# Kernel tuning notes

Hardware: AMD Instinct MI355X
Metric: run time of the kernel (lower is better)

## Reference

```python
import jax, jax.numpy as jnp
import numpy as np

B, S, R, E, H = 2, 2048, 128, 2048, 16
D = E // H  # head_dim = 128


def _ste(x, q):
    # straight-through estimator: forward=q, backward=identity
    return x + jax.lax.stop_gradient(q - x)


def quant_weight(w):
    # BitNet b1.58-style ternary weight quantization with mean-abs scale
    scale = jnp.clip(jnp.mean(jnp.abs(w)), 1e-5, None)
    q = jnp.clip(jnp.round(w / scale), -1.0, 1.0) * scale
    return _ste(w, q)


def quant_act(x):
    # per-token 8-bit absmax activation quantization
    s = 127.0 / jnp.clip(jnp.max(jnp.abs(x), axis=-1, keepdims=True), 1e-5, None)
    q = jnp.clip(jnp.round(x * s), -128.0, 127.0) / s
    return _ste(x, q)


def quantized_linear(x, w):
    # dequantized low-bit matmul: Xq @ Wq^T
    return quant_act(x) @ quant_weight(w).T


def setup_inputs() -> dict:
    key = jax.random.key(0)
    ks = jax.random.split(key, 8)
    sc = 1.0 / np.sqrt(E)
    return {
        "x": jax.random.normal(ks[0], (B, S, E), dtype=jnp.float32),
        "reasoning_tokens": jax.random.normal(ks[1], (B, R, E), dtype=jnp.float32),
        "q_w": jax.random.normal(ks[2], (E, E), dtype=jnp.float32) * sc,
        "k_w": jax.random.normal(ks[3], (E, E), dtype=jnp.float32) * sc,
        "v_w": jax.random.normal(ks[4], (E, E), dtype=jnp.float32) * sc,
        "out_w": jax.random.normal(ks[5], (E, E), dtype=jnp.float32) * sc,
        "out_b": jnp.zeros((E,), dtype=jnp.float32),
    }


def _heads(t):
    b, s, _ = t.shape
    return t.reshape(b, s, H, D).transpose(0, 2, 1, 3)  # [B,H,S,D]


def reference(x, reasoning_tokens, q_w, k_w, v_w, out_w, out_b):
    b, s, e = x.shape
    # quantized QKV projections (dequant + matmul)
    q = _heads(quantized_linear(x, q_w))
    k = _heads(quantized_linear(x, k_w))
    v = _heads(quantized_linear(x, v_w))
    # reasoning tokens go through the UNquantized projections (per source)
    rk = _heads(reasoning_tokens @ k_w.T)
    rv = _heads(reasoning_tokens @ v_w.T)
    k = jnp.concatenate([k, rk], axis=2)  # [B,H,S+R,D]
    v = jnp.concatenate([v, rv], axis=2)
    scores = jnp.einsum('bhqd,bhkd->bhqk', q, k) / np.sqrt(D).astype(np.float32)
    attn = jax.nn.softmax(scores, axis=-1)
    o = jnp.einsum('bhqk,bhkd->bhqd', attn, v)
    o = o.transpose(0, 2, 1, 3).reshape(b, s, e)
    return o @ out_w.T + out_b
```

## Files before the change

kernel.cpp:

```cpp
#include <hip/hip_runtime.h>


typedef __bf16 bf16;
typedef __bf16 bf16x8 __attribute__((ext_vector_type(8)));
typedef float  f32x4  __attribute__((ext_vector_type(4)));

#define B_   2
#define S_   2048
#define R_   128
#define E_   2048
#define H_   16
#define D_   128
#define NKV  2176
#define NTOK 4096
#define MTOT 4352
#define KDIM 2048

typedef const __attribute__((address_space(1))) void* gas_ptr;
typedef __attribute__((address_space(3))) void*       las_ptr;

__device__ __forceinline__ void load_lds16(const void* g, void* l) {
  __builtin_amdgcn_global_load_lds((gas_ptr)g, (las_ptr)l, 16, 0, 0);
}

__global__ __launch_bounds__(256) void abs_sum_k(
    const float* __restrict__ w0, const float* __restrict__ w1,
    const float* __restrict__ w2, double* wsD) {
  int z = blockIdx.y;
  const float* w = z == 0 ? w0 : (z == 1 ? w1 : w2);
  int tid = threadIdx.x;
  size_t base = ((size_t)blockIdx.x * 256 + tid) * 8;
  f32x4 a = *(const f32x4*)(w + base);
  f32x4 b = *(const f32x4*)(w + base + 4);
  float s = 0.f;
#pragma unroll
  for (int j = 0; j < 4; j++) s += fabsf(a[j]) + fabsf(b[j]);
  double d = (double)s;
#pragma unroll
  for (int m = 1; m < 64; m <<= 1) d += __shfl_xor(d, m);
  __shared__ double red[4];
  if ((tid & 63) == 0) red[tid >> 6] = d;
  __syncthreads();
  if (tid == 0) atomicAdd(&wsD[z], red[0] + red[1] + red[2] + red[3]);
}

__global__ __launch_bounds__(256) void ternary_k(
    const float* __restrict__ w0, const float* __restrict__ w1,
    const float* __restrict__ w2, const double* __restrict__ wsD, float* wsF,
    bf16* __restrict__ t0, bf16* __restrict__ t1, bf16* __restrict__ t2) {
  int z = blockIdx.y;
  const float* w = z == 0 ? w0 : (z == 1 ? w1 : w2);
  bf16* t        = z == 0 ? t0 : (z == 1 ? t1 : t2);
  float scale = (float)fmax(wsD[z] * (1.0 / 4194304.0), 1e-5);
  if (blockIdx.x == 0 && threadIdx.x == 0) wsF[z] = scale;
  size_t base = ((size_t)blockIdx.x * 256 + threadIdx.x) * 8;
  f32x4 a = *(const f32x4*)(w + base);
  f32x4 b = *(const f32x4*)(w + base + 4);
  float rs = 1.0f / scale;
  bf16x8 o;
#pragma unroll
  for (int j = 0; j < 8; j++) {
    float v = j < 4 ? a[j] : b[j - 4];
    float q = rintf(v * rs);
    q = fminf(fmaxf(q, -1.f), 1.f);
    o[j] = (bf16)q;
  }
  *(bf16x8*)(t + base) = o;
}

__global__ __launch_bounds__(256) void actq_k(
    const float* __restrict__ x, bf16* __restrict__ xq,
    float* __restrict__ aScale) {
  int row = blockIdx.x, tid = threadIdx.x;
  const float* xr = x + (size_t)row * E_;
  f32x4 a = *(const f32x4*)(xr + tid * 8);
  f32x4 b = *(const f32x4*)(xr + tid * 8 + 4);
  float am = 0.f;
#pragma unroll
  for (int j = 0; j < 4; j++) am = fmaxf(am, fmaxf(fabsf(a[j]), fabsf(b[j])));
#pragma unroll
  for (int m = 1; m < 64; m <<= 1) am = fmaxf(am, __shfl_xor(am, m));
  __shared__ float red[4];
  if ((tid & 63) == 0) red[tid >> 6] = am;
  __syncthreads();
  float mx = fmaxf(fmaxf(red[0], red[1]), fmaxf(red[2], red[3]));
  float maxC = fmaxf(mx, 1e-5f);
  float s = 127.0f / maxC;
  bf16x8 o;
#pragma unroll
  for (int j = 0; j < 8; j++) {
    float v = j < 4 ? a[j] : b[j - 4];
    float q = rintf(v * s);
    q = fminf(fmaxf(q, -128.f), 127.f);
    o[j] = (bf16)q;
  }
  *(bf16x8*)(xq + (size_t)row * E_ + tid * 8) = o;
  if (tid == 0) aScale[row] = maxC / 127.0f;
}

__global__ __launch_bounds__(256) void cvt_k(const float* __restrict__ src,
                                             bf16* __restrict__ dst) {
  size_t i = ((size_t)blockIdx.x * 256 + threadIdx.x) * 8;
  f32x4 a = *(const f32x4*)(src + i);
  f32x4 b = *(const f32x4*)(src + i + 4);
  bf16x8 o;
#pragma unroll
  for (int j = 0; j < 4; j++) { o[j] = (bf16)a[j]; o[j + 4] = (bf16)b[j]; }
  *(bf16x8*)(dst + i) = o;
}

__global__ __launch_bounds__(256) void cvt2_k(const float* __restrict__ s0,
                                              const float* __restrict__ s1,
                                              bf16* __restrict__ d0,
                                              bf16* __restrict__ d1) {
  const float* src = blockIdx.y ? s1 : s0;
  bf16* dst = blockIdx.y ? d1 : d0;
  size_t i = ((size_t)blockIdx.x * 256 + threadIdx.x) * 8;
  f32x4 a = *(const f32x4*)(src + i);
  f32x4 b = *(const f32x4*)(src + i + 4);
  bf16x8 o;
#pragma unroll
  for (int j = 0; j < 4; j++) { o[j] = (bf16)a[j]; o[j + 4] = (bf16)b[j]; }
  *(bf16x8*)(dst + i) = o;
}

__global__ __launch_bounds__(256) void cvt_rt_k(const float* __restrict__ rt,
                                                bf16* __restrict__ dst,
                                                float* __restrict__ asc) {
  int row = blockIdx.x;
  size_t base = (size_t)row * E_;
  int t = threadIdx.x;
  f32x4 a = *(const f32x4*)(rt + base + t * 8);
  f32x4 b = *(const f32x4*)(rt + base + t * 8 + 4);
  bf16x8 o;
#pragma unroll
  for (int j = 0; j < 4; j++) { o[j] = (bf16)a[j]; o[j + 4] = (bf16)b[j]; }
  *(bf16x8*)(dst + (size_t)(NTOK + row) * E_ + t * 8) = o;
  if (t == 0) asc[NTOK + row] = 1.0f;
}

__device__ __forceinline__ void gemm_core(const bf16* Arow, const bf16* Brow,
                                          bf16* As, bf16* Bs, int tid,
                                          f32x4 acc[4][4]) {
  int wave = tid >> 6, lane = tid & 63, quad = lane >> 4, l16 = lane & 15;
  int wm = wave >> 1, wn = wave & 1;
  const char* aT = (const char*)Arow;
  const char* bT = (const char*)Brow;
  int c1 = tid + 256;
  size_t aO0 = (size_t)(tid >> 2) * (KDIM * 2) + (size_t)(tid & 3) * 16;
  size_t aO1 = (size_t)(c1 >> 2) * (KDIM * 2) + (size_t)(c1 & 3) * 16;
  char* AsB = (char*)As;
  char* BsB = (char*)Bs;
  int wofs = wave * 1024;
  for (int k0 = 0; k0 < KDIM; k0 += 32) {
    __syncthreads();
    load_lds16(aT + aO0, AsB + wofs);
    load_lds16(aT + aO1, AsB + 4096 + wofs);
    load_lds16(bT + aO0, BsB + wofs);
    load_lds16(bT + aO1, BsB + 4096 + wofs);
    aT += 64;
    bT += 64;
    __syncthreads();
    bf16x8 af[4], bfr[4];
#pragma unroll
    for (int mt = 0; mt < 4; mt++)
      af[mt] = *(const bf16x8*)(As + (wm * 64 + mt * 16 + l16) * 32 + quad * 8);
#pragma unroll
    for (int nt = 0; nt < 4; nt++)
      bfr[nt] = *(const bf16x8*)(Bs + (wn * 64 + nt * 16 + l16) * 32 + quad * 8);
#pragma unroll
    for (int mt = 0; mt < 4; mt++)
#pragma unroll
      for (int nt = 0; nt < 4; nt++)
        acc[mt][nt] = __builtin_amdgcn_mfma_f32_16x16x32_bf16(
            af[mt], bfr[nt], acc[mt][nt], 0, 0, 0);
  }
}

__global__ __launch_bounds__(256) void gemm_qk(
    const bf16* __restrict__ XQR, const bf16* __restrict__ TQ,
    const bf16* __restrict__ TK, const bf16* __restrict__ KWb,
    const float* __restrict__ asc, const float* __restrict__ wsF,
    bf16* __restrict__ QB, bf16* __restrict__ KB) {
  __shared__ bf16 As[128 * 32];
  __shared__ bf16 Bs[128 * 32];
  int m0 = blockIdx.x * 128, n0 = blockIdx.y * 128;
  bool isQ = n0 < 2048;
  bool isRsn = m0 >= NTOK;
  if (isQ && isRsn) return;
  int tid = threadIdx.x;
  int lane = tid & 63, quad = lane >> 4, l16 = lane & 15;
  int wm = (tid >> 6) >> 1, wn = (tid >> 6) & 1;

  const bf16* Bm = isQ ? (TQ + (size_t)n0 * KDIM)
                       : (isRsn ? (KWb + (size_t)(n0 - 2048) * KDIM)
                                : (TK + (size_t)(n0 - 2048) * KDIM));
  float sW = isQ ? wsF[0] : (isRsn ? 1.0f : wsF[1]);

  f32x4 acc[4][4];
  const f32x4 fz = {0.f, 0.f, 0.f, 0.f};
#pragma unroll
  for (int i = 0; i < 4; i++)
#pragma unroll
    for (int j = 0; j < 4; j++) acc[i][j] = fz;
  gemm_core(XQR + (size_t)m0 * KDIM, Bm, As, Bs, tid, acc);

#pragma unroll
  for (int mt = 0; mt < 4; mt++) {
    int mB = m0 + wm * 64 + mt * 16 + quad * 4;
#pragma unroll
    for (int nt = 0; nt < 4; nt++) {
      int n = n0 + wn * 64 + nt * 16 + l16;
      int nn = n & 2047, h = nn >> 7, d = nn & 127;
#pragma unroll
      for (int r = 0; r < 4; r++) {
        int m = mB + r;
        float v = acc[mt][nt][r] * asc[m] * sW;
        int tb, ts;
        if (isRsn) { int j = m - NTOK; tb = j >> 7; ts = 2048 + (j & 127); }
        else       { tb = m >> 11; ts = m & 2047; }
        if (isQ)
          QB[((size_t)((tb * 16 + h) * S_ + ts)) * 128 + d] = (bf16)v;
        else
          KB[((size_t)((tb * 16 + h) * NKV + ts)) * 128 + d] = (bf16)v;
      }
    }
  }
}

__global__ __launch_bounds__(256) void gemm_vt(
    const bf16* __restrict__ TV, const bf16* __restrict__ VWb,
    const bf16* __restrict__ XQR, const float* __restrict__ asc,
    const float* __restrict__ wsF, bf16* __restrict__ VT) {
  __shared__ bf16 As[128 * 32];
  __shared__ bf16 Bs[128 * 32];
  int m0 = blockIdx.x * 128, n0 = blockIdx.y * 128;
  bool isRsn = n0 >= NTOK;
  int tid = threadIdx.x;
  int lane = tid & 63, quad = lane >> 4, l16 = lane & 15;
  int wm = (tid >> 6) >> 1, wn = (tid >> 6) & 1;

  const bf16* Am = (isRsn ? VWb : TV) + (size_t)m0 * KDIM;
  float sW = isRsn ? 1.0f : wsF[2];

  f32x4 acc[4][4];
  const f32x4 fz = {0.f, 0.f, 0.f, 0.f};
#pragma unroll
  for (int i = 0; i < 4; i++)
#pragma unroll
    for (int j = 0; j < 4; j++) acc[i][j] = fz;
  gemm_core(Am, XQR + (size_t)n0 * KDIM, As, Bs, tid, acc);

#pragma unroll
  for (int mt = 0; mt < 4; mt++) {
    int mB = m0 + wm * 64 + mt * 16 + quad * 4;
#pragma unroll
    for (int nt = 0; nt < 4; nt++) {
      int n = n0 + wn * 64 + nt * 16 + l16;
      float sb = asc[n] * sW;
      int tb, ts;
      if (isRsn) { int j = n - NTOK; tb = j >> 7; ts = 2048 + (j & 127); }
      else       { tb = n >> 11; ts = n & 2047; }
#pragma unroll
      for (int r = 0; r < 4; r++) {
        int m = mB + r, h = m >> 7, d = m & 127;
        VT[((size_t)((tb * 16 + h) * 128 + d)) * NKV + ts] =
            (bf16)(acc[mt][nt][r] * sb);
      }
    }
  }
}

__global__ __launch_bounds__(256) void gemm_out(
    const bf16* __restrict__ A, const bf16* __restrict__ Bm,
    const float* __restrict__ bias, float* __restrict__ out) {
  __shared__ bf16 As[128 * 32];
  __shared__ bf16 Bs[128 * 32];
  int m0 = blockIdx.x * 128, n0 = blockIdx.y * 128;
  int tid = threadIdx.x;
  int lane = tid & 63, quad = lane >> 4, l16 = lane & 15;
  int wm = (tid >> 6) >> 1, wn = (tid >> 6) & 1;

  f32x4 acc[4][4];
  const f32x4 fz = {0.f, 0.f, 0.f, 0.f};
#pragma unroll
  for (int i = 0; i < 4; i++)
#pragma unroll
    for (int j = 0; j < 4; j++) acc[i][j] = fz;
  gemm_core(A + (size_t)m0 * KDIM, Bm + (size_t)n0 * KDIM, As, Bs, tid, acc);

#pragma unroll
  for (int mt = 0; mt < 4; mt++) {
    int mB = m0 + wm * 64 + mt * 16 + quad * 4;
#pragma unroll
    for (int nt = 0; nt < 4; nt++) {
      int n = n0 + wn * 64 + nt * 16 + l16;
      float bv = bias[n];
#pragma unroll
      for (int r = 0; r < 4; r++)
        out[(size_t)(mB + r) * E_ + n] = acc[mt][nt][r] + bv;
    }
  }
}

__global__ __launch_bounds__(256) void attn_k(
    const bf16* __restrict__ q, const bf16* __restrict__ k,
    const bf16* __restrict__ vt, bf16* __restrict__ o) {
  __shared__ bf16 Ks[64 * 128];
  __shared__ bf16 Vs[128 * 64];
  __shared__ bf16 Ps[128 * 64];
  const float SC = 0.08838834764831845f;
  const float SHIFT = 12.0f;
  int tid = threadIdx.x;
  int wave = tid >> 6, lane = tid & 63, quad = lane >> 4, l16 = lane & 15;
  int bh = blockIdx.y, q0 = blockIdx.x * 128;

  const bf16* qb = q + ((size_t)bh * S_ + q0) * D_;
  const char* kb = (const char*)(k + (size_t)bh * NKV * D_);
  const char* vb = (const char*)(vt + (size_t)bh * D_ * NKV);

  bf16x8 qf[2][4];
#pragma unroll
  for (int qt = 0; qt < 2; qt++)
#pragma unroll
    for (int ds = 0; ds < 4; ds++)
      qf[qt][ds] = *(const bf16x8*)(qb +
                   (size_t)(wave * 32 + qt * 16 + l16) * D_ + ds * 32 + quad * 8);

  const f32x4 fz = {0.f, 0.f, 0.f, 0.f};
  f32x4 oa[2][8];
#pragma unroll
  for (int i = 0; i < 2; i++)
#pragma unroll
    for (int j = 0; j < 8; j++) oa[i][j] = fz;
  float lsum[2][4];
#pragma unroll
  for (int i = 0; i < 2; i++)
#pragma unroll
    for (int r = 0; r < 4; r++) lsum[i][r] = 0.f;

  char* KsB = (char*)Ks;
  char* VsB = (char*)Vs;
  char* PsB = (char*)Ps;

  int kRow[4], kC[4], vRow[4], vC[4];
#pragma unroll
  for (int i = 0; i < 4; i++) {
    int slot = i * 256 + tid;
    kRow[i] = slot >> 4;
    kC[i] = (slot & 15) ^ (kRow[i] & 15);
    vRow[i] = slot >> 3;
    vC[i] = (slot & 7) ^ (vRow[i] & 7);
  }
  int wofs = wave * 1024;

  for (int kv = 0; kv < NKV; kv += 64) {
    __syncthreads();
#pragma unroll
    for (int i = 0; i < 4; i++)
      load_lds16(kb + (size_t)(kv + kRow[i]) * 256 + kC[i] * 16,
                 KsB + i * 4096 + wofs);
#pragma unroll
    for (int i = 0; i < 4; i++)
      load_lds16(vb + (size_t)vRow[i] * (NKV * 2) + (size_t)kv * 2 + vC[i] * 16,
                 VsB + i * 4096 + wofs);
    __syncthreads();

    f32x4 s[2][4];
#pragma unroll
    for (int i = 0; i < 2; i++)
#pragma unroll
      for (int j = 0; j < 4; j++) s[i][j] = fz;
#pragma unroll
    for (int ds = 0; ds < 4; ds++) {
      bf16x8 kf[4];
#pragma unroll
      for (int kt = 0; kt < 4; kt++) {
        int row = kt * 16 + l16;
        int c = (ds * 4 + quad) ^ (row & 15);
        kf[kt] = *(const bf16x8*)(KsB + row * 256 + c * 16);
      }
#pragma unroll
      for (int qt = 0; qt < 2; qt++)
#pragma unroll
        for (int kt = 0; kt < 4; kt++)
          s[qt][kt] = __builtin_amdgcn_mfma_f32_16x16x32_bf16(
              qf[qt][ds], kf[kt], s[qt][kt], 0, 0, 0);
    }

#pragma unroll
    for (int qt = 0; qt < 2; qt++)
#pragma unroll
      for (int kt = 0; kt < 4; kt++)
#pragma unroll
        for (int r = 0; r < 4; r++)
          s[qt][kt][r] = __expf(s[qt][kt][r] * SC - SHIFT);
#pragma unroll
    for (int qt = 0; qt < 2; qt++)
#pragma unroll
      for (int r = 0; r < 4; r++)
        lsum[qt][r] += (s[qt][0][r] + s[qt][1][r]) + (s[qt][2][r] + s[qt][3][r]);

#pragma unroll
    for (int qt = 0; qt < 2; qt++)
#pragma unroll
      for (int kt = 0; kt < 4; kt++)
#pragma unroll
        for (int r = 0; r < 4; r++) {
          int row = wave * 32 + qt * 16 + quad * 4 + r;
          int col = kt * 16 + l16;
          int c = (col >> 3) ^ (row & 7);
          *(bf16*)(PsB + row * 128 + c * 16 + (col & 7) * 2) =
              (bf16)s[qt][kt][r];
        }
    __syncthreads();

#pragma unroll
    for (int ks = 0; ks < 2; ks++) {
      bf16x8 pf[2], vf[8];
#pragma unroll
      for (int qt = 0; qt < 2; qt++) {
        int row = wave * 32 + qt * 16 + l16;
        int c = (ks * 4 + quad) ^ (row & 7);
        pf[qt] = *(const bf16x8*)(PsB + row * 128 + c * 16);
      }
#pragma unroll
      for (int dt = 0; dt < 8; dt++) {
        int row = dt * 16 + l16;
        int c = (ks * 4 + quad) ^ (row & 7);
        vf[dt] = *(const bf16x8*)(VsB + row * 128 + c * 16);
      }
#pragma unroll
      for (int qt = 0; qt < 2; qt++)
#pragma unroll
        for (int dt = 0; dt < 8; dt++)
          oa[qt][dt] = __builtin_amdgcn_mfma_f32_16x16x32_bf16(
              pf[qt], vf[dt], oa[qt][dt], 0, 0, 0);
    }
  }

  int b = bh >> 4, h = bh & 15;
#pragma unroll
  for (int qt = 0; qt < 2; qt++) {
    float rl[4];
#pragma unroll
    for (int r = 0; r < 4; r++) {
      float l = lsum[qt][r];
#pragma unroll
      for (int msk = 1; msk < 16; msk <<= 1) l += __shfl_xor(l, msk);
      rl[r] = 1.0f / l;
    }
#pragma unroll
    for (int dt = 0; dt < 8; dt++)
#pragma unroll
      for (int r = 0; r < 4; r++) {
        int srow = q0 + wave * 32 + qt * 16 + quad * 4 + r;
        int col = h * 128 + dt * 16 + l16;
        o[((size_t)(b * S_ + srow)) * E_ + col] = (bf16)(oa[qt][dt][r] * rl[r]);
      }
  }
}

static constexpr size_t O_ASC  = 256;
static constexpr size_t O_XQR  = 32768;
static constexpr size_t SZ_XQR = (size_t)MTOT * E_ * 2;
static constexpr size_t SZ_W   = (size_t)E_ * E_ * 2;
static constexpr size_t O_TQ   = O_XQR + SZ_XQR;
static constexpr size_t O_TK   = O_TQ + SZ_W;
static constexpr size_t O_TV   = O_TK + SZ_W;
static constexpr size_t O_KWB  = O_TV + SZ_W;
static constexpr size_t O_VWB  = O_KWB + SZ_W;
static constexpr size_t O_QB   = O_VWB + SZ_W;
static constexpr size_t SZ_QB  = (size_t)B_ * H_ * S_ * D_ * 2;
static constexpr size_t O_KB   = O_QB + SZ_QB;
static constexpr size_t SZ_KB  = (size_t)B_ * H_ * NKV * D_ * 2;
static constexpr size_t O_VT   = O_KB + SZ_KB;
static constexpr size_t O_OB   = O_TQ;
static constexpr size_t O_OWB  = O_KWB;
static constexpr size_t WS_NEED = O_VT + SZ_KB;

extern "C" void kernel_launch(void* const* d_in, const int* in_sizes, int n_in,
                              void* d_out, int out_size, void* d_ws,
                              size_t ws_size, hipStream_t stream) {
  const float* x  = (const float*)d_in[0];
  const float* rt = (const float*)d_in[1];
  const float* qw = (const float*)d_in[2];
  const float* kw = (const float*)d_in[3];
  const float* vw = (const float*)d_in[4];
  const float* ow = (const float*)d_in[5];
  const float* ob = (const float*)d_in[6];
  char* ws = (char*)d_ws;
  if (ws_size < WS_NEED) return;

  double* wsD = (double*)ws;
  float* wsF  = (float*)(ws + 64);
  float* asc  = (float*)(ws + O_ASC);
  bf16* XQR = (bf16*)(ws + O_XQR);
  bf16* TQ  = (bf16*)(ws + O_TQ);
  bf16* TK  = (bf16*)(ws + O_TK);
  bf16* TV  = (bf16*)(ws + O_TV);
  bf16* KWb = (bf16*)(ws + O_KWB);
  bf16* VWb = (bf16*)(ws + O_VWB);
  bf16* QB  = (bf16*)(ws + O_QB);
  bf16* KB  = (bf16*)(ws + O_KB);
  bf16* VT  = (bf16*)(ws + O_VT);
  bf16* OB  = (bf16*)(ws + O_OB);
  bf16* OWb = (bf16*)(ws + O_OWB);
  float* out = (float*)d_out;

  hipMemsetAsync(ws, 0, 64, stream);
  abs_sum_k<<<dim3(2048, 3), 256, 0, stream>>>(qw, kw, vw, wsD);
  ternary_k<<<dim3(2048, 3), 256, 0, stream>>>(qw, kw, vw, wsD, wsF, TQ, TK, TV);
  actq_k<<<4096, 256, 0, stream>>>(x, XQR, asc);
  cvt_rt_k<<<256, 256, 0, stream>>>(rt, XQR, asc);
  cvt2_k<<<dim3(2048, 2), 256, 0, stream>>>(kw, vw, KWb, VWb);

  gemm_qk<<<dim3(34, 32), 256, 0, stream>>>(XQR, TQ, TK, KWb, asc, wsF, QB, KB);
  cvt_k<<<2048, 256, 0, stream>>>(ow, OWb);
  gemm_vt<<<dim3(16, 34), 256, 0, stream>>>(TV, VWb, XQR, asc, wsF, VT);

  attn_k<<<dim3(16, 32), 256, 0, stream>>>(QB, KB, VT, OB);

  gemm_out<<<dim3(32, 16), 256, 0, stream>>>(OB, OWb, ob, out);
}
```

Before: 581.5 us.

## Use int8 MFMA for quantized QKV projections and fuse prep kernels

Quantized activations and ternary weights are now stored as int8 instead of bf16, and the quantized Q/K/V projections use the i8 16x16x64 MFMA with a swizzled LDS layout, which halves operand bytes and doubles the k-step per instruction. Reasoning-token projections keep a separate bf16 path since they are unquantized. The weight ternarization and all fp32-to-bf16 conversions are merged into one prep kernel, cutting launches. Exactness relies on int32 accumulation of integer products, which matches the dequantized reference up to rounding order.

```diff
diff --git a/kernel.cpp b/kernel.cpp
--- a/kernel.cpp
+++ b/kernel.cpp
@@ -4,6 +4,8 @@
 typedef __bf16 bf16;
 typedef __bf16 bf16x8 __attribute__((ext_vector_type(8)));
 typedef float  f32x4  __attribute__((ext_vector_type(4)));
+typedef int    i32x4  __attribute__((ext_vector_type(4)));
+typedef char   char8  __attribute__((ext_vector_type(8)));
 
 #define B_   2
 #define S_   2048
@@ -13,7 +15,6 @@
 #define D_   128
 #define NKV  2176
 #define NTOK 4096
-#define MTOT 4352
 #define KDIM 2048
 
 typedef const __attribute__((address_space(1))) void* gas_ptr;
@@ -44,32 +45,48 @@
   if (tid == 0) atomicAdd(&wsD[z], red[0] + red[1] + red[2] + red[3]);
 }
 
-__global__ __launch_bounds__(256) void ternary_k(
-    const float* __restrict__ w0, const float* __restrict__ w1,
-    const float* __restrict__ w2, const double* __restrict__ wsD, float* wsF,
-    bf16* __restrict__ t0, bf16* __restrict__ t1, bf16* __restrict__ t2) {
-  int z = blockIdx.y;
-  const float* w = z == 0 ? w0 : (z == 1 ? w1 : w2);
-  bf16* t        = z == 0 ? t0 : (z == 1 ? t1 : t2);
-  float scale = (float)fmax(wsD[z] * (1.0 / 4194304.0), 1e-5);
-  if (blockIdx.x == 0 && threadIdx.x == 0) wsF[z] = scale;
-  size_t base = ((size_t)blockIdx.x * 256 + threadIdx.x) * 8;
-  f32x4 a = *(const f32x4*)(w + base);
-  f32x4 b = *(const f32x4*)(w + base + 4);
-  float rs = 1.0f / scale;
-  bf16x8 o;
-#pragma unroll
-  for (int j = 0; j < 8; j++) {
-    float v = j < 4 ? a[j] : b[j - 4];
-    float q = rintf(v * rs);
-    q = fminf(fmaxf(q, -1.f), 1.f);
-    o[j] = (bf16)q;
-  }
-  *(bf16x8*)(t + base) = o;
+__global__ __launch_bounds__(256) void prep_k(
+    const float* __restrict__ qw, const float* __restrict__ kw,
+    const float* __restrict__ vw, const float* __restrict__ ow,
+    const float* __restrict__ rt, const double* __restrict__ wsD, float* wsF,
+    char* __restrict__ TQ8, char* __restrict__ TK8, char* __restrict__ TV8,
+    bf16* __restrict__ KWb, bf16* __restrict__ VWb, bf16* __restrict__ OWb,
+    bf16* __restrict__ RTb) {
+  int y = blockIdx.y;
+  if (y < 3) {
+    const float* w = y == 0 ? qw : (y == 1 ? kw : vw);
+    char* t        = y == 0 ? TQ8 : (y == 1 ? TK8 : TV8);
+    float scale = (float)fmax(wsD[y] * (1.0 / 4194304.0), 1e-5);
+    if (blockIdx.x == 0 && threadIdx.x == 0) wsF[y] = scale;
+    size_t base = ((size_t)blockIdx.x * 256 + threadIdx.x) * 8;
+    f32x4 a = *(const f32x4*)(w + base);
+    f32x4 b = *(const f32x4*)(w + base + 4);
+    float rs = 1.0f / scale;
+    char8 o;
+#pragma unroll
+    for (int j = 0; j < 8; j++) {
+      float v = j < 4 ? a[j] : b[j - 4];
+      float q = rintf(v * rs);
+      q = fminf(fmaxf(q, -1.f), 1.f);
+      o[j] = (char)(int)q;
+    }
+    *(char8*)(t + base) = o;
+  } else {
+    if (y == 6 && blockIdx.x >= 256) return;
+    const float* src = y == 3 ? kw : (y == 4 ? vw : (y == 5 ? ow : rt));
+    bf16* dst        = y == 3 ? KWb : (y == 4 ? VWb : (y == 5 ? OWb : RTb));
+    size_t i = ((size_t)blockIdx.x * 256 + threadIdx.x) * 8;
+    f32x4 a = *(const f32x4*)(src + i);
+    f32x4 b = *(const f32x4*)(src + i + 4);
+    bf16x8 o;
+#pragma unroll
+    for (int j = 0; j < 4; j++) { o[j] = (bf16)a[j]; o[j + 4] = (bf16)b[j]; }
+    *(bf16x8*)(dst + i) = o;
+  }
 }
 
 __global__ __launch_bounds__(256) void actq_k(
-    const float* __restrict__ x, bf16* __restrict__ xq,
+    const float* __restrict__ x, char* __restrict__ xq,
     float* __restrict__ aScale) {
   int row = blockIdx.x, tid = threadIdx.x;
   const float* xr = x + (size_t)row * E_;
@@ -86,57 +103,16 @@
   float mx = fmaxf(fmaxf(red[0], red[1]), fmaxf(red[2], red[3]));
   float maxC = fmaxf(mx, 1e-5f);
   float s = 127.0f / maxC;
-  bf16x8 o;
+  char8 o;
 #pragma unroll
   for (int j = 0; j < 8; j++) {
     float v = j < 4 ? a[j] : b[j - 4];
     float q = rintf(v * s);
     q = fminf(fmaxf(q, -128.f), 127.f);
-    o[j] = (bf16)q;
-  }
-  *(bf16x8*)(xq + (size_t)row * E_ + tid * 8) = o;
+    o[j] = (char)(int)q;
+  }
+  *(char8*)(xq + (size_t)row * E_ + tid * 8) = o;
   if (tid == 0) aScale[row] = maxC / 127.0f;
-}
-
-__global__ __launch_bounds__(256) void cvt_k(const float* __restrict__ src,
-                                             bf16* __restrict__ dst) {
-  size_t i = ((size_t)blockIdx.x * 256 + threadIdx.x) * 8;
-  f32x4 a = *(const f32x4*)(src + i);
-  f32x4 b = *(const f32x4*)(src + i + 4);
-  bf16x8 o;
-#pragma unroll
-  for (int j = 0; j < 4; j++) { o[j] = (bf16)a[j]; o[j + 4] = (bf16)b[j]; }
-  *(bf16x8*)(dst + i) = o;
-}
-
-__global__ __launch_bounds__(256) void cvt2_k(const float* __restrict__ s0,
-                                              const float* __restrict__ s1,
-                                              bf16* __restrict__ d0,
-                                              bf16* __restrict__ d1) {
-  const float* src = blockIdx.y ? s1 : s0;
-  bf16* dst = blockIdx.y ? d1 : d0;
-  size_t i = ((size_t)blockIdx.x * 256 + threadIdx.x) * 8;
-  f32x4 a = *(const f32x4*)(src + i);
-  f32x4 b = *(const f32x4*)(src + i + 4);
-  bf16x8 o;
-#pragma unroll
-  for (int j = 0; j < 4; j++) { o[j] = (bf16)a[j]; o[j + 4] = (bf16)b[j]; }
-  *(bf16x8*)(dst + i) = o;
-}
-
-__global__ __launch_bounds__(256) void cvt_rt_k(const float* __restrict__ rt,
-                                                bf16* __restrict__ dst,
-                                                float* __restrict__ asc) {
-  int row = blockIdx.x;
-  size_t base = (size_t)row * E_;
-  int t = threadIdx.x;
-  f32x4 a = *(const f32x4*)(rt + base + t * 8);
-  f32x4 b = *(const f32x4*)(rt + base + t * 8 + 4);
-  bf16x8 o;
-#pragma unroll
-  for (int j = 0; j < 4; j++) { o[j] = (bf16)a[j]; o[j + 4] = (bf16)b[j]; }
-  *(bf16x8*)(dst + (size_t)(NTOK + row) * E_ + t * 8) = o;
-  if (t == 0) asc[NTOK + row] = 1.0f;
 }
 
 __device__ __forceinline__ void gemm_core(const bf16* Arow, const bf16* Brow,
@@ -177,13 +153,52 @@
   }
 }
 
+__device__ __forceinline__ void gemm_core_i8(const char* Arow, const char* Brow,
+                                             char* As, char* Bs, int tid,
+                                             i32x4 acc[4][4]) {
+  int wave = tid >> 6, lane = tid & 63, quad = lane >> 4, l16 = lane & 15;
+  int wm = wave >> 1, wn = wave & 1;
+  int s0 = tid, s1 = tid + 256;
+  int r0 = s0 >> 2, r1 = s1 >> 2;
+  size_t aO0 = (size_t)r0 * KDIM + (size_t)((s0 & 3) ^ (r0 & 3)) * 16;
+  size_t aO1 = (size_t)r1 * KDIM + (size_t)((s1 & 3) ^ (r1 & 3)) * 16;
+  const char* aT = Arow;
+  const char* bT = Brow;
+  int wofs = wave * 1024;
+  int cs = (quad ^ (l16 & 3)) * 16;
+  for (int k0 = 0; k0 < KDIM; k0 += 64) {
+    __syncthreads();
+    load_lds16(aT + aO0, As + wofs);
+    load_lds16(aT + aO1, As + 4096 + wofs);
+    load_lds16(bT + aO0, Bs + wofs);
+    load_lds16(bT + aO1, Bs + 4096 + wofs);
+    aT += 64;
+    bT += 64;
+    __syncthreads();
+    i32x4 af[4], bfr[4];
+#pragma unroll
+    for (int mt = 0; mt < 4; mt++)
+      af[mt] = *(const i32x4*)(As + (wm * 64 + mt * 16 + l16) * 64 + cs);
+#pragma unroll
+    for (int nt = 0; nt < 4; nt++)
+      bfr[nt] = *(const i32x4*)(Bs + (wn * 64 + nt * 16 + l16) * 64 + cs);
+#pragma unroll
+    for (int mt = 0; mt < 4; mt++)
+#pragma unroll
+      for (int nt = 0; nt < 4; nt++)
+        acc[mt][nt] = __builtin_amdgcn_mfma_i32_16x16x64_i8(
+            af[mt], bfr[nt], acc[mt][nt], 0, 0, 0);
+  }
+}
+
 __global__ __launch_bounds__(256) void gemm_qk(
-    const bf16* __restrict__ XQR, const bf16* __restrict__ TQ,
-    const bf16* __restrict__ TK, const bf16* __restrict__ KWb,
-    const float* __restrict__ asc, const float* __restrict__ wsF,
-    bf16* __restrict__ QB, bf16* __restrict__ KB) {
-  __shared__ bf16 As[128 * 32];
-  __shared__ bf16 Bs[128 * 32];
+    const char* __restrict__ XQ8, const char* __restrict__ TQ8,
+    const char* __restrict__ TK8, const bf16* __restrict__ RTb,
+    const bf16* __restrict__ KWb, const float* __restrict__ asc,
+    const float* __restrict__ wsF, bf16* __restrict__ QB,
+    bf16* __restrict__ KB) {
+  __shared__ char As[8192];
+  __shared__ char Bs[8192];
   int m0 = blockIdx.x * 128, n0 = blockIdx.y * 128;
   bool isQ = n0 < 2048;
   bool isRsn = m0 >= NTOK;
@@ -192,80 +207,124 @@
   int lane = tid & 63, quad = lane >> 4, l16 = lane & 15;
   int wm = (tid >> 6) >> 1, wn = (tid >> 6) & 1;
 
-  const bf16* Bm = isQ ? (TQ + (size_t)n0 * KDIM)
-                       : (isRsn ? (KWb + (size_t)(n0 - 2048) * KDIM)
-                                : (TK + (size_t)(n0 - 2048) * KDIM));
-  float sW = isQ ? wsF[0] : (isRsn ? 1.0f : wsF[1]);
-
-  f32x4 acc[4][4];
-  const f32x4 fz = {0.f, 0.f, 0.f, 0.f};
-#pragma unroll
-  for (int i = 0; i < 4; i++)
-#pragma unroll
-    for (int j = 0; j < 4; j++) acc[i][j] = fz;
-  gemm_core(XQR + (size_t)m0 * KDIM, Bm, As, Bs, tid, acc);
-
-#pragma unroll
-  for (int mt = 0; mt < 4; mt++) {
-    int mB = m0 + wm * 64 + mt * 16 + quad * 4;
-#pragma unroll
-    for (int nt = 0; nt < 4; nt++) {
-      int n = n0 + wn * 64 + nt * 16 + l16;
-      int nn = n & 2047, h = nn >> 7, d = nn & 127;
-#pragma unroll
-      for (int r = 0; r < 4; r++) {
-        int m = mB + r;
-        float v = acc[mt][nt][r] * asc[m] * sW;
-        int tb, ts;
-        if (isRsn) { int j = m - NTOK; tb = j >> 7; ts = 2048 + (j & 127); }
-        else       { tb = m >> 11; ts = m & 2047; }
-        if (isQ)
-          QB[((size_t)((tb * 16 + h) * S_ + ts)) * 128 + d] = (bf16)v;
-        else
-          KB[((size_t)((tb * 16 + h) * NKV + ts)) * 128 + d] = (bf16)v;
+  if (!isRsn) {
+    const char* Bm = isQ ? (TQ8 + (size_t)n0 * KDIM)
+                         : (TK8 + (size_t)(n0 - 2048) * KDIM);
+    float sW = isQ ? wsF[0] : wsF[1];
+    i32x4 acc[4][4];
+    const i32x4 iz = {0, 0, 0, 0};
+#pragma unroll
+    for (int i = 0; i < 4; i++)
+#pragma unroll
+      for (int j = 0; j < 4; j++) acc[i][j] = iz;
+    gemm_core_i8(XQ8 + (size_t)m0 * KDIM, Bm, As, Bs, tid, acc);
+#pragma unroll
+    for (int mt = 0; mt < 4; mt++) {
+      int mB = m0 + wm * 64 + mt * 16 + quad * 4;
+#pragma unroll
+      for (int nt = 0; nt < 4; nt++) {
+        int n = n0 + wn * 64 + nt * 16 + l16;
+        int nn = n & 2047, h = nn >> 7, d = nn & 127;
+#pragma unroll
+        for (int r = 0; r < 4; r++) {
+          int m = mB + r;
+          float v = (float)acc[mt][nt][r] * asc[m] * sW;
+          int tb = m >> 11, ts = m & 2047;
+          if (isQ)
+            QB[((size_t)((tb * 16 + h) * S_ + ts)) * 128 + d] = (bf16)v;
+          else
+            KB[((size_t)((tb * 16 + h) * NKV + ts)) * 128 + d] = (bf16)v;
+        }
+      }
+    }
+  } else {
+    f32x4 acc[4][4];
+    const f32x4 fz = {0.f, 0.f, 0.f, 0.f};
+#pragma unroll
+    for (int i = 0; i < 4; i++)
+#pragma unroll
+      for (int j = 0; j < 4; j++) acc[i][j] = fz;
+    gemm_core(RTb + (size_t)(m0 - NTOK) * KDIM,
+              KWb + (size_t)(n0 - 2048) * KDIM, (bf16*)As, (bf16*)Bs, tid, acc);
+#pragma unroll
+    for (int mt = 0; mt < 4; mt++) {
+      int mB = m0 + wm * 64 + mt * 16 + quad * 4;
+#pragma unroll
+      for (int nt = 0; nt < 4; nt++) {
+        int n = n0 + wn * 64 + nt * 16 + l16;
+        int nn = n & 2047, h = nn >> 7, d = nn & 127;
+#pragma unroll
+        for (int r = 0; r < 4; r++) {
+          int j = mB + r - NTOK;
+          int tb = j >> 7, ts = 2048 + (j & 127);
+          KB[((size_t)((tb * 16 + h) * NKV + ts)) * 128 + d] =
+              (bf16)acc[mt][nt][r];
+        }
       }
     }
   }
 }
 
 __global__ __launch_bounds__(256) void gemm_vt(
-    const bf16* __restrict__ TV, const bf16* __restrict__ VWb,
-    const bf16* __restrict__ XQR, const float* __restrict__ asc,
-    const float* __restrict__ wsF, bf16* __restrict__ VT) {
-  __shared__ bf16 As[128 * 32];
-  __shared__ bf16 Bs[128 * 32];
+    const char* __restrict__ TV8, const char* __restrict__ XQ8,
+    const bf16* __restrict__ VWb, const bf16* __restrict__ RTb,
+    const float* __restrict__ asc, const float* __restrict__ wsF,
+    bf16* __restrict__ VT) {
+  __shared__ char As[8192];
+  __shared__ char Bs[8192];
   int m0 = blockIdx.x * 128, n0 = blockIdx.y * 128;
   bool isRsn = n0 >= NTOK;
   int tid = threadIdx.x;
   int lane = tid & 63, quad = lane >> 4, l16 = lane & 15;
   int wm = (tid >> 6) >> 1, wn = (tid >> 6) & 1;
 
-  const bf16* Am = (isRsn ? VWb : TV) + (size_t)m0 * KDIM;
-  float sW = isRsn ? 1.0f : wsF[2];
-
-  f32x4 acc[4][4];
-  const f32x4 fz = {0.f, 0.f, 0.f, 0.f};
-#pragma unroll
-  for (int i = 0; i < 4; i++)
-#pragma unroll
-    for (int j = 0; j < 4; j++) acc[i][j] = fz;
-  gemm_core(Am, XQR + (size_t)n0 * KDIM, As, Bs, tid, acc);
-
-#pragma unroll
-  for (int mt = 0; mt < 4; mt++) {
-    int mB = m0 + wm * 64 + mt * 16 + quad * 4;
-#pragma unroll
-    for (int nt = 0; nt < 4; nt++) {
-      int n = n0 + wn * 64 + nt * 16 + l16;
-      float sb = asc[n] * sW;
-      int tb, ts;
-      if (isRsn) { int j = n - NTOK; tb = j >> 7; ts = 2048 + (j & 127); }
-      else       { tb = n >> 11; ts = n & 2047; }
-#pragma unroll
-      for (int r = 0; r < 4; r++) {
-        int m = mB + r, h = m >> 7, d = m & 127;
-        VT[((size_t)((tb * 16 + h) * 128 + d)) * NKV + ts] =
-            (bf16)(acc[mt][nt][r] * sb);
+  if (!isRsn) {
+    i32x4 acc[4][4];
+    const i32x4 iz = {0, 0, 0, 0};
+#pragma unroll
+    for (int i = 0; i < 4; i++)
+#pragma unroll
+      for (int j = 0; j < 4; j++) acc[i][j] = iz;
+    gemm_core_i8(TV8 + (size_t)m0 * KDIM, XQ8 + (size_t)n0 * KDIM, As, Bs,
+                 tid, acc);
+#pragma unroll
+    for (int mt = 0; mt < 4; mt++) {
+      int mB = m0 + wm * 64 + mt * 16 + quad * 4;
+#pragma unroll
+      for (int nt = 0; nt < 4; nt++) {
+        int n = n0 + wn * 64 + nt * 16 + l16;
+        float sb = asc[n] * wsF[2];
+        int tb = n >> 11, ts = n & 2047;
+#pragma unroll
+        for (int r = 0; r < 4; r++) {
+          int m = mB + r, h = m >> 7, d = m & 127;
+          VT[((size_t)((tb * 16 + h) * 128 + d)) * NKV + ts] =
+              (bf16)((float)acc[mt][nt][r] * sb);
+        }
+      }
+    }
+  } else {
+    f32x4 acc[4][4];
+    const f32x4 fz = {0.f, 0.f, 0.f, 0.f};
+#pragma unroll
+    for (int i = 0; i < 4; i++)
+#pragma unroll
+      for (int j = 0; j < 4; j++) acc[i][j] = fz;
+    gemm_core(VWb + (size_t)m0 * KDIM, RTb + (size_t)(n0 - NTOK) * KDIM,
+              (bf16*)As, (bf16*)Bs, tid, acc);
+#pragma unroll
+    for (int mt = 0; mt < 4; mt++) {
+      int mB = m0 + wm * 64 + mt * 16 + quad * 4;
+#pragma unroll
+      for (int nt = 0; nt < 4; nt++) {
+        int n = n0 + wn * 64 + nt * 16 + l16;
+        int j = n - NTOK, tb = j >> 7, ts = 2048 + (j & 127);
+#pragma unroll
+        for (int r = 0; r < 4; r++) {
+          int m = mB + r, h = m >> 7, d = m & 127;
+          VT[((size_t)((tb * 16 + h) * 128 + d)) * NKV + ts] =
+              (bf16)acc[mt][nt][r];
+        }
       }
     }
   }
@@ -461,23 +520,20 @@
   }
 }
 
-static constexpr size_t O_ASC  = 256;
-static constexpr size_t O_XQR  = 32768;
-static constexpr size_t SZ_XQR = (size_t)MTOT * E_ * 2;
-static constexpr size_t SZ_W   = (size_t)E_ * E_ * 2;
-static constexpr size_t O_TQ   = O_XQR + SZ_XQR;
-static constexpr size_t O_TK   = O_TQ + SZ_W;
-static constexpr size_t O_TV   = O_TK + SZ_W;
-static constexpr size_t O_KWB  = O_TV + SZ_W;
-static constexpr size_t O_VWB  = O_KWB + SZ_W;
-static constexpr size_t O_QB   = O_VWB + SZ_W;
-static constexpr size_t SZ_QB  = (size_t)B_ * H_ * S_ * D_ * 2;
-static constexpr size_t O_KB   = O_QB + SZ_QB;
-static constexpr size_t SZ_KB  = (size_t)B_ * H_ * NKV * D_ * 2;
-static constexpr size_t O_VT   = O_KB + SZ_KB;
-static constexpr size_t O_OB   = O_TQ;
-static constexpr size_t O_OWB  = O_KWB;
-static constexpr size_t WS_NEED = O_VT + SZ_KB;
+static constexpr size_t O_ASC = 256;
+static constexpr size_t O_XQ8 = 32768;
+static constexpr size_t O_RTB = O_XQ8 + 8388608;
+static constexpr size_t O_TQ8 = O_RTB + 1048576;
+static constexpr size_t O_TK8 = O_TQ8 + 4194304;
+static constexpr size_t O_TV8 = O_TK8 + 4194304;
+static constexpr size_t O_KWB = O_TV8 + 4194304;
+static constexpr size_t O_VWB = O_KWB + 8388608;
+static constexpr size_t O_OWB = O_VWB + 8388608;
+static constexpr size_t O_QB  = O_OWB + 8388608;
+static constexpr size_t O_KB  = O_QB + 16777216;
+static constexpr size_t O_VT  = O_KB + 17825792;
+static constexpr size_t O_OB  = O_XQ8;
+static constexpr size_t WS_NEED = O_VT + 17825792;
 
 extern "C" void kernel_launch(void* const* d_in, const int* in_sizes, int n_in,
                               void* d_out, int out_size, void* d_ws,
@@ -495,29 +551,29 @@
   double* wsD = (double*)ws;
   float* wsF  = (float*)(ws + 64);
   float* asc  = (float*)(ws + O_ASC);
-  bf16* XQR = (bf16*)(ws + O_XQR);
-  bf16* TQ  = (bf16*)(ws + O_TQ);
-  bf16* TK  = (bf16*)(ws + O_TK);
-  bf16* TV  = (bf16*)(ws + O_TV);
+  char* XQ8 = ws + O_XQ8;
+  bf16* RTb = (bf16*)(ws + O_RTB);
+  char* TQ8 = ws + O_TQ8;
+  char* TK8 = ws + O_TK8;
+  char* TV8 = ws + O_TV8;
   bf16* KWb = (bf16*)(ws + O_KWB);
   bf16* VWb = (bf16*)(ws + O_VWB);
+  bf16* OWb = (bf16*)(ws + O_OWB);
   bf16* QB  = (bf16*)(ws + O_QB);
   bf16* KB  = (bf16*)(ws + O_KB);
   bf16* VT  = (bf16*)(ws + O_VT);
   bf16* OB  = (bf16*)(ws + O_OB);
-  bf16* OWb = (bf16*)(ws + O_OWB);
   float* out = (float*)d_out;
 
   hipMemsetAsync(ws, 0, 64, stream);
   abs_sum_k<<<dim3(2048, 3), 256, 0, stream>>>(qw, kw, vw, wsD);
-  ternary_k<<<dim3(2048, 3), 256, 0, stream>>>(qw, kw, vw, wsD, wsF, TQ, TK, TV);
-  actq_k<<<4096, 256, 0, stream>>>(x, XQR, asc);
-  cvt_rt_k<<<256, 256, 0, stream>>>(rt, XQR, asc);
-  cvt2_k<<<dim3(2048, 2), 256, 0, stream>>>(kw, vw, KWb, VWb);
-
-  gemm_qk<<<dim3(34, 32), 256, 0, stream>>>(XQR, TQ, TK, KWb, asc, wsF, QB, KB);
-  cvt_k<<<2048, 256, 0, stream>>>(ow, OWb);
-  gemm_vt<<<dim3(16, 34), 256, 0, stream>>>(TV, VWb, XQR, asc, wsF, VT);
+  prep_k<<<dim3(2048, 7), 256, 0, stream>>>(qw, kw, vw, ow, rt, wsD, wsF,
+                                            TQ8, TK8, TV8, KWb, VWb, OWb, RTb);
+  actq_k<<<4096, 256, 0, stream>>>(x, XQ8, asc);
+
+  gemm_qk<<<dim3(34, 32), 256, 0, stream>>>(XQ8, TQ8, TK8, RTb, KWb, asc, wsF,
+                                            QB, KB);
+  gemm_vt<<<dim3(16, 34), 256, 0, stream>>>(TV8, XQ8, VWb, RTb, asc, wsF, VT);
 
   attn_k<<<dim3(16, 32), 256, 0, stream>>>(QB, KB, VT, OB);
 
```

Result: faster. 558.2 us (-4.0%).
